# Optimization experiments

Measured on AMD Instinct MI355X. Metric: run time of the kernel, lower is better.

Reference implementation:

```python
import jax, jax.numpy as jnp
import numpy as np

MARGIN = 0.3
BIG = 1e30  # finite sentinel for masked max/min (avoids inf-inf NaNs)


def setup_inputs() -> dict:
    key = jax.random.key(0)
    k1, k2 = jax.random.split(key)
    N, D = 8192, 128
    embeddings = jax.random.normal(k1, (N, D), dtype=jnp.float32)
    labels = jax.random.randint(k2, (N,), 0, 1024, dtype=jnp.int64)
    return {"embeddings": embeddings, "labels": labels}


def _pairwise_euclidean(x):
    # torch.cdist(x, x, p=2): sqrt of clamped squared distances,
    # with a double-where so sqrt(0) has no NaN gradient.
    sq = jnp.sum(x * x, axis=1)                      # [N]
    d2 = sq[:, None] + sq[None, :] - 2.0 * (x @ x.T)  # [N, N]
    d2 = jnp.maximum(d2, 0.0)
    safe = jnp.where(d2 > 0.0, d2, 1.0)
    return jnp.where(d2 > 0.0, jnp.sqrt(safe), 0.0)


def reference(embeddings, labels):
    dist = _pairwise_euclidean(embeddings)           # [N, N]
    same = labels[:, None] == labels[None, :]        # [N, N]
    eye = jnp.eye(labels.shape[0], dtype=bool)
    mask_pos = same & ~eye
    mask_neg = ~same

    hardest_pos = jnp.max(jnp.where(mask_pos, dist, -BIG), axis=1)  # [N]
    hardest_neg = jnp.min(jnp.where(mask_neg, dist, BIG), axis=1)   # [N]

    valid = jnp.any(mask_pos, axis=1) & jnp.any(mask_neg, axis=1)
    per_row = jax.nn.relu(hardest_pos - hardest_neg + MARGIN)
    per_row = jnp.where(valid, per_row, 0.0)
    cnt = jnp.sum(valid.astype(jnp.float32))
    # torch code returns 0.0 when no valid anchors
    return jnp.where(cnt > 0, jnp.sum(per_row) / jnp.maximum(cnt, 1.0), 0.0)
```

## Files before the change

kernel.cpp:

```cpp
#include <hip/hip_runtime.h>
#include <hip/hip_bf16.h>

#define NSPLIT 16
#define BIGF 1e30f
#define MARGIN 0.3f
#define DK 128

typedef __attribute__((ext_vector_type(8))) short bf16x8;
typedef __attribute__((ext_vector_type(4))) float f32x4;

#define WS_HIST 0
#define WS_HP   1024
#define WS_HN   (1024 + 8192)
#define WS_GSUM (1024 + 16384)
#define WS_GCNT (WS_GSUM + 1)
#define WS_BCNT (WS_GSUM + 2)
#define WS_SQ   (WS_GSUM + 4)
#define WS_XB   (WS_SQ + 8192)


__global__ void prep_kernel(const float* __restrict__ x, ushort* __restrict__ xs,
                            float* __restrict__ sq, unsigned* __restrict__ hist,
                            const int* __restrict__ lab, int N) {
    int wave = threadIdx.x >> 6;
    int lane = threadIdx.x & 63;
    int row = blockIdx.x * 4 + wave;
    if (row >= N) return;
    const float2* xr = (const float2*)(x + (size_t)row * DK);
    float2 v = xr[lane];
    __hip_bfloat16 b0 = __float2bfloat16(v.x);
    __hip_bfloat16 b1 = __float2bfloat16(v.y);
    ushort2 st;
    st.x = *(ushort*)&b0;
    st.y = *(ushort*)&b1;
    size_t off = (size_t)(row >> 4) * 2048 + (size_t)(lane >> 2) * 128
               + (size_t)(row & 15) * 8 + 2 * (lane & 3);
    *(ushort2*)(xs + off) = st;
    float s = v.x * v.x + v.y * v.y;
    #pragma unroll
    for (int o = 32; o > 0; o >>= 1) s += __shfl_xor(s, o, 64);
    if (lane == 0) {
        sq[row] = s;
        atomicAdd(&hist[lab[row]], 1u);
    }
}

__global__ __launch_bounds__(256, 2) void tile_kernel(
    const ushort* __restrict__ xs, const float* __restrict__ sq,
    const int* __restrict__ lab,
    unsigned* __restrict__ hp_bits, unsigned* __restrict__ hn_comp, int N)
{
    __shared__ ushort a_s[128 * DK];
    __shared__ int   laba_s[128];
    __shared__ float red_hp[128][2];
    __shared__ float red_hn[128][2];

    const int tid  = threadIdx.x;
    const int lane = tid & 63;
    const int wave = tid >> 6;
    const int m16  = lane & 15;
    const int quad = lane >> 4;
    const int rbase = blockIdx.x * 128;
    const int wrow = (wave >> 1) * 64;
    const int wcol = (wave & 1) * 64;

    {
        const bf16x8* srcv = (const bf16x8*)(xs + (size_t)rbase * DK);
        bf16x8* dstv = (bf16x8*)a_s;
        #pragma unroll
        for (int i = 0; i < 8; ++i)
            dstv[tid + i * 256] = srcv[tid + i * 256];
    }
    if (tid < 128) laba_s[tid] = lab[rbase + tid];
    __syncthreads();

    int rlab[4][4];
    #pragma unroll
    for (int mt = 0; mt < 4; ++mt)
        #pragma unroll
        for (int r = 0; r < 4; ++r)
            rlab[mt][r] = laba_s[wrow + mt * 16 + quad * 4 + r];

    float runhp[4][4], runhn[4][4];
    #pragma unroll
    for (int mt = 0; mt < 4; ++mt)
        #pragma unroll
        for (int r = 0; r < 4; ++r) { runhp[mt][r] = -BIGF; runhn[mt][r] = BIGF; }

    const ushort* a_base = a_s + (size_t)((wave >> 1) * 4) * 2048
                         + (size_t)quad * 128 + (size_t)m16 * 8;

    const int cols_per_split = N / NSPLIT;
    const int cbegin = blockIdx.y * cols_per_split;

    for (int ci = 0; ci < cols_per_split; ci += 128) {
        const int cbase = cbegin + ci + wcol;
        const ushort* b_base = xs + (size_t)cbase * DK
                             + (size_t)quad * 128 + (size_t)m16 * 8;

        #pragma unroll 1
        for (int h = 0; h < 2; ++h) {
            float sqbv[2]; int lbv[2];
            #pragma unroll
            for (int j = 0; j < 2; ++j) {
                int colg = cbase + (h * 2 + j) * 16 + m16;
                sqbv[j] = sq[colg];
                lbv[j]  = lab[colg];
            }

            f32x4 acc[4][2];
            #pragma unroll
            for (int mt = 0; mt < 4; ++mt)
                #pragma unroll
                for (int j = 0; j < 2; ++j)
                    acc[mt][j] = (f32x4){0.f, 0.f, 0.f, 0.f};

            #pragma unroll
            for (int s = 0; s < 4; ++s) {
                bf16x8 bfr[2], afr[4];
                #pragma unroll
                for (int j = 0; j < 2; ++j)
                    bfr[j] = *(const bf16x8*)(b_base + (size_t)(h * 2 + j) * 2048 + s * 512);
                #pragma unroll
                for (int mt = 0; mt < 4; ++mt)
                    afr[mt] = *(const bf16x8*)(a_base + mt * 2048 + s * 512);
                #pragma unroll
                for (int mt = 0; mt < 4; ++mt)
                    #pragma unroll
                    for (int j = 0; j < 2; ++j)
                        acc[mt][j] = __builtin_amdgcn_mfma_f32_16x16x32_bf16(
                            afr[mt], bfr[j], acc[mt][j], 0, 0, 0);
            }

            #pragma unroll
            for (int j = 0; j < 2; ++j) {
                #pragma unroll
                for (int mt = 0; mt < 4; ++mt) {
                    #pragma unroll
                    for (int r = 0; r < 4; ++r) {
                        float t = fmaf(-2.0f, acc[mt][j][r], sqbv[j]);
                        bool same = (rlab[mt][r] == lbv[j]);
                        runhp[mt][r] = fmaxf(runhp[mt][r], same ? t : -BIGF);
                        runhn[mt][r] = fminf(runhn[mt][r], same ? BIGF : t);
                    }
                }
            }
        }
    }

    #pragma unroll
    for (int mt = 0; mt < 4; ++mt)
        #pragma unroll
        for (int r = 0; r < 4; ++r) {
            #pragma unroll
            for (int o = 8; o > 0; o >>= 1) {
                runhp[mt][r] = fmaxf(runhp[mt][r], __shfl_xor(runhp[mt][r], o, 16));
                runhn[mt][r] = fminf(runhn[mt][r], __shfl_xor(runhn[mt][r], o, 16));
            }
        }

    if (m16 == 0) {
        #pragma unroll
        for (int mt = 0; mt < 4; ++mt)
            #pragma unroll
            for (int r = 0; r < 4; ++r) {
                int rowl = wrow + mt * 16 + quad * 4 + r;
                red_hp[rowl][wave & 1] = runhp[mt][r];
                red_hn[rowl][wave & 1] = runhn[mt][r];
            }
    }
    __syncthreads();
    if (tid < 128) {
        float thp = fmaxf(red_hp[tid][0], red_hp[tid][1]);
        float thn = fminf(red_hn[tid][0], red_hn[tid][1]);
        float sqa = sq[rbase + tid];
        float d2p = fmaxf(sqa + thp, 0.0f);
        float d2n = fmaxf(sqa + thn, 0.0f);
        atomicMax(&hp_bits[rbase + tid], __float_as_uint(d2p));
        atomicMax(&hn_comp[rbase + tid], ~__float_as_uint(d2n));
    }
}

__global__ void finalize_kernel(const unsigned* __restrict__ hp_bits,
                                const unsigned* __restrict__ hn_comp,
                                const int* __restrict__ lab,
                                const unsigned* __restrict__ hist,
                                float* __restrict__ gsum, float* __restrict__ gcnt,
                                unsigned* __restrict__ bcount,
                                float* __restrict__ out, int N)
{
    __shared__ float s_sum[256];
    __shared__ float s_cnt[256];
    int tid = threadIdx.x;
    int row = blockIdx.x * 256 + tid;
    float loss = 0.0f, cv = 0.0f;
    if (row < N) {
        unsigned c = hist[lab[row]];
        bool valid = (c >= 2u) && (c < (unsigned)N);
        if (valid) {
            float dp = sqrtf(__uint_as_float(hp_bits[row]));
            float dn = sqrtf(__uint_as_float(~hn_comp[row]));
            loss = fmaxf(dp - dn + MARGIN, 0.0f);
            cv = 1.0f;
        }
    }
    s_sum[tid] = loss; s_cnt[tid] = cv;
    __syncthreads();
    for (int o = 128; o > 0; o >>= 1) {
        if (tid < o) { s_sum[tid] += s_sum[tid + o]; s_cnt[tid] += s_cnt[tid + o]; }
        __syncthreads();
    }
    if (tid == 0) {
        atomicAdd(gsum, s_sum[0]);
        atomicAdd(gcnt, s_cnt[0]);
        __threadfence();
        unsigned old = atomicAdd(bcount, 1u);
        if (old == gridDim.x - 1) {
            float s = atomicAdd(gsum, 0.0f);
            float c = atomicAdd(gcnt, 0.0f);
            out[0] = (c > 0.0f) ? s / c : 0.0f;
        }
    }
}

extern "C" void kernel_launch(void* const* d_in, const int* in_sizes, int n_in,
                              void* d_out, int out_size, void* d_ws, size_t ws_size,
                              hipStream_t stream) {
    const float* x = (const float*)d_in[0];
    const int* lab = (const int*)d_in[1];
    float* out = (float*)d_out;
    const int N = in_sizes[1];

    unsigned* ws = (unsigned*)d_ws;
    unsigned* hist    = ws + WS_HIST;
    unsigned* hp_bits = ws + WS_HP;
    unsigned* hn_comp = ws + WS_HN;
    float* gsum = (float*)(ws + WS_GSUM);
    float* gcnt = (float*)(ws + WS_GCNT);
    unsigned* bcount = ws + WS_BCNT;
    float* sq = (float*)(ws + WS_SQ);
    ushort* xs = (ushort*)(ws + WS_XB);

    hipMemsetAsync(d_ws, 0, (size_t)WS_SQ * sizeof(unsigned), stream);
    prep_kernel<<<N / 4, 256, 0, stream>>>(x, xs, sq, hist, lab, N);
    dim3 grid(N / 128, NSPLIT);
    tile_kernel<<<grid, 256, 0, stream>>>(xs, sq, lab, hp_bits, hn_comp, N);
    finalize_kernel<<<N / 256, 256, 0, stream>>>(hp_bits, hn_comp, lab, hist,
                                                 gsum, gcnt, bcount, out, N);
}
```

Before: 101.6 us.

## Prefetch B fragments into registers, restructure prep, shrink memset

```diff
diff --git a/kernel.cpp b/kernel.cpp
--- a/kernel.cpp
+++ b/kernel.cpp
@@ -10,40 +10,101 @@
 typedef __attribute__((ext_vector_type(4))) float f32x4;
 
 #define WS_HIST 0
-#define WS_HP   1024
-#define WS_HN   (1024 + 8192)
-#define WS_GSUM (1024 + 16384)
-#define WS_GCNT (WS_GSUM + 1)
-#define WS_BCNT (WS_GSUM + 2)
-#define WS_SQ   (WS_GSUM + 4)
+#define WS_GSUM 1024
+#define WS_GCNT 1025
+#define WS_BCNT 1026
+#define WS_HP   1028
+#define WS_HN   (WS_HP + 8192)
+#define WS_SQ   (WS_HN + 8192)
 #define WS_XB   (WS_SQ + 8192)
-
-
-__global__ void prep_kernel(const float* __restrict__ x, ushort* __restrict__ xs,
-                            float* __restrict__ sq, unsigned* __restrict__ hist,
-                            const int* __restrict__ lab, int N) {
-    int wave = threadIdx.x >> 6;
-    int lane = threadIdx.x & 63;
-    int row = blockIdx.x * 4 + wave;
-    if (row >= N) return;
-    const float2* xr = (const float2*)(x + (size_t)row * DK);
-    float2 v = xr[lane];
-    __hip_bfloat16 b0 = __float2bfloat16(v.x);
-    __hip_bfloat16 b1 = __float2bfloat16(v.y);
-    ushort2 st;
-    st.x = *(ushort*)&b0;
-    st.y = *(ushort*)&b1;
-    size_t off = (size_t)(row >> 4) * 2048 + (size_t)(lane >> 2) * 128
-               + (size_t)(row & 15) * 8 + 2 * (lane & 3);
-    *(ushort2*)(xs + off) = st;
-    float s = v.x * v.x + v.y * v.y;
-    #pragma unroll
-    for (int o = 32; o > 0; o >>= 1) s += __shfl_xor(s, o, 64);
-    if (lane == 0) {
+#define WS_ZERO_BYTES (1028 * 4)
+
+
+__global__ __launch_bounds__(256) void prep_kernel(
+    const float* __restrict__ x, ushort* __restrict__ xs,
+    float* __restrict__ sq, unsigned* __restrict__ hist,
+    const int* __restrict__ lab,
+    unsigned* __restrict__ hp_bits, unsigned* __restrict__ hn_comp, int N)
+{
+    __shared__ float part[32][17];
+    const int tid = threadIdx.x;
+    const int rbase = blockIdx.x * 32;
+    const int rlq = tid & 15;
+    const int kc  = tid >> 4;
+    bf16x8* outv = (bf16x8*)(xs + (size_t)rbase * DK);
+
+    #pragma unroll
+    for (int g = 0; g < 2; ++g) {
+        int row = rbase + g * 16 + rlq;
+        const float4* p = (const float4*)(x + (size_t)row * DK + kc * 8);
+        float4 u = p[0], v = p[1];
+        float f[8] = {u.x, u.y, u.z, u.w, v.x, v.y, v.z, v.w};
+        union { bf16x8 v8; ushort us[8]; } o;
+        float ps = 0.0f;
+        #pragma unroll
+        for (int e = 0; e < 8; ++e) {
+            __hip_bfloat16 b = __float2bfloat16(f[e]);
+            o.us[e] = *(ushort*)&b;
+            ps += f[e] * f[e];
+        }
+        outv[g * 256 + tid] = o.v8;
+        part[g * 16 + rlq][kc] = ps;
+    }
+    __syncthreads();
+    if (tid < 32) {
+        float s = 0.0f;
+        #pragma unroll
+        for (int k = 0; k < 16; ++k) s += part[tid][k];
+        int row = rbase + tid;
         sq[row] = s;
+        hp_bits[row] = 0u;
+        hn_comp[row] = 0u;
         atomicAdd(&hist[lab[row]], 1u);
     }
 }
+
+
+#define ZERO_ACC(ACC)                                                     \
+    _Pragma("unroll")                                                     \
+    for (int mt = 0; mt < 4; ++mt)                                        \
+        _Pragma("unroll")                                                 \
+        for (int j = 0; j < 2; ++j)                                       \
+            ACC[mt][j] = (f32x4){0.f, 0.f, 0.f, 0.f};
+
+#define MFMA_HALF(ACC, B)                                                 \
+    _Pragma("unroll")                                                     \
+    for (int s = 0; s < 4; ++s) {                                         \
+        bf16x8 afr[4];                                                    \
+        _Pragma("unroll")                                                 \
+        for (int mt = 0; mt < 4; ++mt)                                    \
+            afr[mt] = *(const bf16x8*)(a_base + mt * 2048 + s * 512);     \
+        _Pragma("unroll")                                                 \
+        for (int mt = 0; mt < 4; ++mt)                                    \
+            _Pragma("unroll")                                             \
+            for (int j = 0; j < 2; ++j)                                   \
+                ACC[mt][j] = __builtin_amdgcn_mfma_f32_16x16x32_bf16(     \
+                    afr[mt], B[j][s], ACC[mt][j], 0, 0, 0);               \
+    }
+
+#define EPI_HALF(ACC, SQB, LB)                                            \
+    _Pragma("unroll")                                                     \
+    for (int mt = 0; mt < 4; ++mt) {                                      \
+        int4 rl4 = *(const int4*)&laba_s[wrow + mt * 16 + quad * 4];      \
+        const int rla[4] = {rl4.x, rl4.y, rl4.z, rl4.w};                  \
+        _Pragma("unroll")                                                 \
+        for (int r = 0; r < 4; ++r) {                                     \
+            float t0 = fmaf(-2.0f, ACC[mt][0][r], SQB[0]);                \
+            float t1 = fmaf(-2.0f, ACC[mt][1][r], SQB[1]);                \
+            bool s0 = (rla[r] == LB[0]);                                  \
+            bool s1 = (rla[r] == LB[1]);                                  \
+            float cp0 = s0 ? t0 : -BIGF;                                  \
+            float cp1 = s1 ? t1 : -BIGF;                                  \
+            runhp[mt][r] = fmaxf(fmaxf(runhp[mt][r], cp0), cp1);          \
+            float cn0 = s0 ? BIGF : t0;                                   \
+            float cn1 = s1 ? BIGF : t1;                                   \
+            runhn[mt][r] = fminf(fminf(runhn[mt][r], cn0), cn1);          \
+        }                                                                 \
+    }
 
 __global__ __launch_bounds__(256, 2) void tile_kernel(
     const ushort* __restrict__ xs, const float* __restrict__ sq,
@@ -74,78 +135,62 @@
     if (tid < 128) laba_s[tid] = lab[rbase + tid];
     __syncthreads();
 
-    int rlab[4][4];
+    float runhp[4][4], runhn[4][4];
     #pragma unroll
     for (int mt = 0; mt < 4; ++mt)
         #pragma unroll
-        for (int r = 0; r < 4; ++r)
-            rlab[mt][r] = laba_s[wrow + mt * 16 + quad * 4 + r];
-
-    float runhp[4][4], runhn[4][4];
-    #pragma unroll
-    for (int mt = 0; mt < 4; ++mt)
-        #pragma unroll
         for (int r = 0; r < 4; ++r) { runhp[mt][r] = -BIGF; runhn[mt][r] = BIGF; }
 
-    const ushort* a_base = a_s + (size_t)((wave >> 1) * 4) * 2048
-                         + (size_t)quad * 128 + (size_t)m16 * 8;
+    const ushort* a_base = a_s + wrow * DK + quad * 128 + m16 * 8;
 
     const int cols_per_split = N / NSPLIT;
-    const int cbegin = blockIdx.y * cols_per_split;
-
+    const int cbegin = blockIdx.y * cols_per_split + wcol;
+
+    unsigned voff[4];
+    #pragma unroll
+    for (int c = 0; c < 4; ++c)
+        voff[c] = (unsigned)(cbegin + c * 16) * DK + quad * 128 + m16 * 8;
+
+    #pragma unroll 1
     for (int ci = 0; ci < cols_per_split; ci += 128) {
-        const int cbase = cbegin + ci + wcol;
-        const ushort* b_base = xs + (size_t)cbase * DK
-                             + (size_t)quad * 128 + (size_t)m16 * 8;
-
-        #pragma unroll 1
-        for (int h = 0; h < 2; ++h) {
-            float sqbv[2]; int lbv[2];
-            #pragma unroll
-            for (int j = 0; j < 2; ++j) {
-                int colg = cbase + (h * 2 + j) * 16 + m16;
-                sqbv[j] = sq[colg];
-                lbv[j]  = lab[colg];
-            }
-
-            f32x4 acc[4][2];
-            #pragma unroll
-            for (int mt = 0; mt < 4; ++mt)
-                #pragma unroll
-                for (int j = 0; j < 2; ++j)
-                    acc[mt][j] = (f32x4){0.f, 0.f, 0.f, 0.f};
-
-            #pragma unroll
-            for (int s = 0; s < 4; ++s) {
-                bf16x8 bfr[2], afr[4];
-                #pragma unroll
-                for (int j = 0; j < 2; ++j)
-                    bfr[j] = *(const bf16x8*)(b_base + (size_t)(h * 2 + j) * 2048 + s * 512);
-                #pragma unroll
-                for (int mt = 0; mt < 4; ++mt)
-                    afr[mt] = *(const bf16x8*)(a_base + mt * 2048 + s * 512);
-                #pragma unroll
-                for (int mt = 0; mt < 4; ++mt)
-                    #pragma unroll
-                    for (int j = 0; j < 2; ++j)
-                        acc[mt][j] = __builtin_amdgcn_mfma_f32_16x16x32_bf16(
-                            afr[mt], bfr[j], acc[mt][j], 0, 0, 0);
-            }
-
-            #pragma unroll
-            for (int j = 0; j < 2; ++j) {
-                #pragma unroll
-                for (int mt = 0; mt < 4; ++mt) {
-                    #pragma unroll
-                    for (int r = 0; r < 4; ++r) {
-                        float t = fmaf(-2.0f, acc[mt][j][r], sqbv[j]);
-                        bool same = (rlab[mt][r] == lbv[j]);
-                        runhp[mt][r] = fmaxf(runhp[mt][r], same ? t : -BIGF);
-                        runhn[mt][r] = fminf(runhn[mt][r], same ? BIGF : t);
-                    }
-                }
-            }
-        }
+        bf16x8 b0[2][4];
+        #pragma unroll
+        for (int j = 0; j < 2; ++j)
+            #pragma unroll
+            for (int s = 0; s < 4; ++s)
+                b0[j][s] = *(const bf16x8*)(xs + voff[j] + s * 512);
+        float sqb0[2]; int lb0[2];
+        #pragma unroll
+        for (int j = 0; j < 2; ++j) {
+            int colg = cbegin + ci + j * 16 + m16;
+            sqb0[j] = sq[colg]; lb0[j] = lab[colg];
+        }
+
+        f32x4 acc[4][2];
+        ZERO_ACC(acc);
+        MFMA_HALF(acc, b0);
+
+        bf16x8 b1[2][4];
+        #pragma unroll
+        for (int j = 0; j < 2; ++j)
+            #pragma unroll
+            for (int s = 0; s < 4; ++s)
+                b1[j][s] = *(const bf16x8*)(xs + voff[2 + j] + s * 512);
+        float sqb1[2]; int lb1[2];
+        #pragma unroll
+        for (int j = 0; j < 2; ++j) {
+            int colg = cbegin + ci + (2 + j) * 16 + m16;
+            sqb1[j] = sq[colg]; lb1[j] = lab[colg];
+        }
+
+        EPI_HALF(acc, sqb0, lb0);
+
+        ZERO_ACC(acc);
+        MFMA_HALF(acc, b1);
+        EPI_HALF(acc, sqb1, lb1);
+
+        #pragma unroll
+        for (int c = 0; c < 4; ++c) voff[c] += 128 * DK;
     }
 
     #pragma unroll
@@ -233,16 +278,16 @@
 
     unsigned* ws = (unsigned*)d_ws;
     unsigned* hist    = ws + WS_HIST;
-    unsigned* hp_bits = ws + WS_HP;
-    unsigned* hn_comp = ws + WS_HN;
     float* gsum = (float*)(ws + WS_GSUM);
     float* gcnt = (float*)(ws + WS_GCNT);
     unsigned* bcount = ws + WS_BCNT;
+    unsigned* hp_bits = ws + WS_HP;
+    unsigned* hn_comp = ws + WS_HN;
     float* sq = (float*)(ws + WS_SQ);
     ushort* xs = (ushort*)(ws + WS_XB);
 
-    hipMemsetAsync(d_ws, 0, (size_t)WS_SQ * sizeof(unsigned), stream);
-    prep_kernel<<<N / 4, 256, 0, stream>>>(x, xs, sq, hist, lab, N);
+    hipMemsetAsync(d_ws, 0, (size_t)WS_ZERO_BYTES, stream);
+    prep_kernel<<<N / 32, 256, 0, stream>>>(x, xs, sq, hist, lab, hp_bits, hn_comp, N);
     dim3 grid(N / 128, NSPLIT);
     tile_kernel<<<grid, 256, 0, stream>>>(xs, sq, lab, hp_bits, hn_comp, N);
     finalize_kernel<<<N / 256, 256, 0, stream>>>(hp_bits, hn_comp, lab, hist,
```

New measurement: 97.35 us. 1.04x faster.
